# Kernel optimization log

Measured on AMD Instinct MI355X. Metric: run time of the kernel, lower is better.

Reference implementation:

```python
import jax, jax.numpy as jnp
import numpy as np
from functools import partial

EPS = 1e-5
TOP_K = 1
NUM_EXPERTS = 3
LOSS_COEF = 0.01


def conv2d(x, w, stride, pad):
    return jax.lax.conv_general_dilated(
        x, w, (stride, stride), [(pad, pad), (pad, pad)],
        dimension_numbers=("NCHW", "OIHW", "NCHW"))


def setup_inputs() -> dict:
    key = jax.random.key(0)
    ks = jax.random.split(key, 8)
    b, c, t, h, w = 8, 3, 5, 512, 512
    E = NUM_EXPERTS
    s = 0.05  # small init scale
    return {
        "x": jax.random.normal(ks[0], (b, c, t, h, w), jnp.float32),
        "g_conv_w": jax.random.normal(ks[1], (64, 15, 7, 7), jnp.float32) * s,
        "g_bn_gamma": jnp.ones((64,), jnp.float32),
        "g_bn_beta": jnp.zeros((64,), jnp.float32),
        "g_bn_mean": jnp.zeros((64,), jnp.float32),
        "g_bn_var": jnp.ones((64,), jnp.float32),
        "g_fc_w": jax.random.normal(ks[2], (E, 64), jnp.float32) * s,
        "g_fc_b": jnp.zeros((E,), jnp.float32),
        "e_conv1_w": jax.random.normal(ks[3], (E, 64, 15, 7, 7), jnp.float32) * s,
        "e_conv2_w": jax.random.normal(ks[4], (E, 128, 64, 3, 3), jnp.float32) * s,
        "e_head_w1": jax.random.normal(ks[5], (E, 128, 128, 3, 3), jnp.float32) * s,
        "e_head_b1": jnp.zeros((E, 128), jnp.float32),
        "e_head_w2": jax.random.normal(ks[6], (E, 5, 128, 1, 1), jnp.float32) * s,
        "e_head_b2": jnp.zeros((E, 5), jnp.float32),
    }


def gating(xr, g_conv_w, g_bn_gamma, g_bn_beta, g_bn_mean, g_bn_var, g_fc_w, g_fc_b):
    # backbone: conv 7x7 s2 -> BN (eval) -> ReLU -> maxpool 3x3 s2 -> GAP -> fc
    f = conv2d(xr, g_conv_w, 2, 3)
    scale = g_bn_gamma / jnp.sqrt(g_bn_var + EPS)
    f = f * scale[None, :, None, None] + (g_bn_beta - g_bn_mean * scale)[None, :, None, None]
    f = jax.nn.relu(f)
    f = jax.lax.reduce_window(f, -jnp.inf, jax.lax.max, (1, 1, 3, 3), (1, 1, 2, 2),
                              [(0, 0), (0, 0), (1, 1), (1, 1)])
    pooled = f.mean(axis=(2, 3))                       # (b, 64)
    logits = pooled @ g_fc_w.T + g_fc_b                # (b, E)
    b = logits.shape[0]
    _, top_idx = jax.lax.top_k(logits, TOP_K)          # (b, k)
    rows = jnp.arange(b)[:, None]
    # eval-mode gating: uniform 1/k over selected experts
    sparse_gates = jnp.zeros_like(logits).at[rows, top_idx].set(1.0 / TOP_K)
    expert_mask = jnp.zeros_like(logits).at[rows, top_idx].set(1.0)
    density = expert_mask.mean(axis=0)
    density_proxy = jax.nn.softmax(logits, axis=1).mean(axis=0)
    aux_loss = (density * density_proxy).sum() * NUM_EXPERTS
    return sparse_gates, aux_loss


def expert_forward(xr, w1, w2, hw1, hb1, hw2, hb2):
    y = jax.nn.relu(conv2d(xr, w1, 2, 3))              # (b, 64, H/2, W/2)
    y = jax.nn.relu(conv2d(y, w2, 2, 1))               # (b, 128, H/4, W/4)
    y = jax.nn.relu(conv2d(y, hw1, 1, 1) + hb1[None, :, None, None])
    y = conv2d(y, hw2, 1, 0) + hb2[None, :, None, None]  # (b, 5, H/4, W/4)
    return y


def reference(x, g_conv_w, g_bn_gamma, g_bn_beta, g_bn_mean, g_bn_var, g_fc_w, g_fc_b,
              e_conv1_w, e_conv2_w, e_head_w1, e_head_b1, e_head_w2, e_head_b2):
    b, c, t, h, w = x.shape
    xr = x.reshape(b, c * t, h, w)
    sparse_gates, aux_loss = gating(xr, g_conv_w, g_bn_gamma, g_bn_beta,
                                    g_bn_mean, g_bn_var, g_fc_w, g_fc_b)
    # run all experts (gates are 0 for unselected -> identical math to sparse dispatch)
    outs = jax.vmap(lambda w1, w2, hw1, hb1, hw2, hb2:
                    expert_forward(xr, w1, w2, hw1, hb1, hw2, hb2))(
        e_conv1_w, e_conv2_w, e_head_w1, e_head_b1, e_head_w2, e_head_b2)  # (E,b,5,h4,w4)
    combined = jnp.einsum("ebchw,be->bchw", outs, sparse_gates)
    hm, wh, reg = combined[:, 0:1], combined[:, 1:3], combined[:, 3:5]
    return hm, wh, reg, LOSS_COEF * aux_loss
```

## Files before the change

### kernel.cpp

```cpp
#include <hip/hip_runtime.h>
#include <cstdint>
#include <cmath>


typedef _Float16 f16x8 __attribute__((ext_vector_type(8)));
typedef _Float16 f16x4 __attribute__((ext_vector_type(4)));
typedef float f32x4 __attribute__((ext_vector_type(4)));

__device__ __forceinline__ void g2l16(const void* g, void* l) {
  __builtin_amdgcn_global_load_lds((__attribute__((address_space(1))) void*)g,
                                   (__attribute__((address_space(3))) void*)l,
                                   16, 0, 0);
}

__device__ __forceinline__ int xcd_swz(int bid, int nwg) {
  return (bid & 7) * (nwg >> 3) + (bid >> 3);
}

__global__ __launch_bounds__(256) void prep_x_k(
    const float* __restrict__ x, _Float16* __restrict__ xp)
{
  __shared__ __align__(16) _Float16 st[16384];
  const int tid = threadIdx.x;
  const int b   = blockIdx.x >> 8;
  const int blk = blockIdx.x & 255;
  const int px0 = blk * 1024;
  const float* src = x + (size_t)b * 15 * 262144 + px0 + tid * 4;

  f16x8 lo[4], hi[4];
#pragma unroll
  for (int j = 0; j < 4; ++j) hi[j][7] = (_Float16)0.f;
#pragma unroll
  for (int c = 0; c < 15; ++c) {
    const float4 v = *(const float4*)&src[(size_t)c * 262144];
    if (c < 8) {
      lo[0][c] = (_Float16)v.x; lo[1][c] = (_Float16)v.y;
      lo[2][c] = (_Float16)v.z; lo[3][c] = (_Float16)v.w;
    } else {
      hi[0][c - 8] = (_Float16)v.x; hi[1][c - 8] = (_Float16)v.y;
      hi[2][c - 8] = (_Float16)v.z; hi[3][c - 8] = (_Float16)v.w;
    }
  }
#pragma unroll
  for (int j = 0; j < 4; ++j) {
#pragma unroll
    for (int h = 0; h < 2; ++h) {
      const int g  = (tid * 4 + j) * 2 + h;
      const int gs = g ^ ((g >> 3) & 7);
      *(f16x8*)&st[gs * 8] = h ? hi[j] : lo[j];
    }
  }
  __syncthreads();
  _Float16* dst = xp + ((size_t)b * 262144 + px0) * 16;
#pragma unroll
  for (int m = 0; m < 4; ++m) {
    const int px = m * 256 + tid;
#pragma unroll
    for (int h = 0; h < 2; ++h) {
      const int g  = px * 2 + h;
      const int gs = g ^ ((g >> 3) & 7);
      *(f16x8*)&dst[(size_t)px * 16 + h * 8] = *(const f16x8*)&st[gs * 8];
    }
  }
}

__global__ __launch_bounds__(256) void prep_w7_k(
    const float* __restrict__ gw, const float* __restrict__ ew,
    _Float16* __restrict__ wp)
{
  const int i = blockIdx.x * 256 + threadIdx.x;
  const int kk   = i & 31;
  const int cout = (i >> 5) & 63;
  const int pair = (i >> 11) & 3;
  const int v    = i >> 13;
  const int ky = v % 7, set = v / 7;
  const int t = kk >> 4, cin = kk & 15;
  const int kx = 2 * pair + t;
  float val = 0.f;
  if (cin < 15 && kx < 7) {
    if (set == 0) val = gw[((cout * 15 + cin) * 7 + ky) * 7 + kx];
    else          val = ew[((((set - 1) * 64 + cout) * 15 + cin) * 7 + ky) * 7 + kx];
  }
  wp[i] = (_Float16)val;
}

template<int CINC>
__global__ __launch_bounds__(256) void prep_w3_k(
    const float* __restrict__ w, _Float16* __restrict__ wp)
{
  constexpr int CH = CINC / 32;
  const int i = blockIdx.x * 256 + threadIdx.x;
  const int kk   = i & 31;
  const int cout = (i >> 5) & 127;
  int rest = i >> 12;
  const int ch  = rest % CH;  rest /= CH;
  const int tap = rest % 9;
  const int e   = rest / 9;
  const int cin = ch * 32 + kk;
  wp[i] = (_Float16)w[((size_t)(e * 128 + cout) * CINC + cin) * 9 + tap];
}

template<int MODE, int SWZ>
__global__ __launch_bounds__(256, 3) void conv7m_k(
    const _Float16* __restrict__ xp, const _Float16* __restrict__ wp,
    const float* __restrict__ bn_g, const float* __restrict__ bn_b,
    const float* __restrict__ bn_m, const float* __restrict__ bn_v,
    const int* __restrict__ sel, _Float16* __restrict__ out)
{
  constexpr int ROWF = 518 * 16;
  __shared__ __align__(16) _Float16 smem[18432];
  const int sb = SWZ ? xcd_swz(blockIdx.x, 2048) : (int)blockIdx.x;
  const int oy = sb & 255, b = sb >> 8;
  const int wv = threadIdx.x >> 6, lane = threadIdx.x & 63;
  const int ln15 = lane & 15, quad = lane >> 4;
  const int npx0 = wv * 64;

  int set = 0;
  if constexpr (MODE == 1) set = 1 + sel[b];
  const _Float16* wset = wp + (size_t)set * (7 * 4 * 64 * 32);
  const _Float16* xb   = xp + (size_t)b * (512 * 512 * 16);

  const _Float16* xrow[7];
  bool rowok[7];
#pragma unroll
  for (int ky = 0; ky < 7; ++ky) {
    const int iy = 2 * oy - 3 + ky;
    rowok[ky] = (unsigned)iy < 512u;
    const int iyc = iy < 0 ? 0 : (iy > 511 ? 511 : iy);
    xrow[ky] = xb + (size_t)iyc * (512 * 16);
  }

  if (threadIdx.x < 32) {
    const int bi = threadIdx.x >> 4, k = threadIdx.x & 15;
    if (k < 12) {
      const int g = (k < 6) ? k : (1030 + k - 6);
      f16x8 z = {};
      *(f16x8*)&smem[bi * ROWF + g * 8] = z;
    }
  }

  f32x4 acc[4][4];
#pragma unroll
  for (int f = 0; f < 4; ++f)
#pragma unroll
    for (int g = 0; g < 4; ++g) acc[f][g] = (f32x4){0.f, 0.f, 0.f, 0.f};

  auto load_af = [&](int t, f16x8* af) {
    const int ky = t >> 2, pair = t & 3;
    const _Float16* wt = wset + (size_t)((ky * 4 + pair) * 64) * 32;
#pragma unroll
    for (int f = 0; f < 4; ++f)
      af[f] = *(const f16x8*)&wt[(f * 16 + ln15) * 32 + quad * 8];
  };
  auto stage = [&](int ky, int bi) {
    _Float16* bufb = &smem[bi * ROWF];
    const _Float16* xr = xrow[ky];
#pragma unroll
    for (int s = 0; s < 4; ++s) {
      const int seg = wv * 4 + s;
      const int gl = 6 + seg * 64 + lane;
      const int gs = gl ^ ((gl >> 3) & 7);
      g2l16(xr + (size_t)((gs >> 1) - 3) * 16 + (gs & 1) * 8,
            bufb + (6 + seg * 64) * 8);
    }
  };

  int gb[4];
#pragma unroll
  for (int g = 0; g < 4; ++g)
    gb[g] = 4 * (npx0 + g * 16 + ln15) + quad;

  f16x8 afA[4], afB[4];
  load_af(0, afA);
  stage(0, 0);
  __syncthreads();

#pragma unroll
  for (int t = 0; t < 28; ++t) {
    const int ky = t >> 2, pair = t & 3;
    const int cur = ky & 1;
    f16x8* afc = (t & 1) ? afB : afA;
    f16x8* afn = (t & 1) ? afA : afB;
    if (t + 1 < 28) load_af(t + 1, afn);
    if (pair == 0 && ky + 1 < 7) stage(ky + 1, cur ^ 1);
    if (rowok[ky]) {
      const _Float16* bufb = &smem[cur * ROWF];
      __builtin_amdgcn_s_setprio(1);
#pragma unroll
      for (int g = 0; g < 4; ++g) {
        const int gq = gb[g] + 4 * pair;
        const int gs = gq ^ ((gq >> 3) & 7);
        const f16x8 bf = *(const f16x8*)&bufb[gs * 8];
#pragma unroll
        for (int f = 0; f < 4; ++f)
          acc[f][g] = __builtin_amdgcn_mfma_f32_16x16x32_f16(afc[f], bf, acc[f][g], 0, 0, 0);
      }
      __builtin_amdgcn_s_setprio(0);
    }
    if (pair == 3) __syncthreads();
  }

  _Float16* sw = &smem[wv * 4608];
#pragma unroll
  for (int f = 0; f < 4; ++f) {
    float scl[4], add[4];
#pragma unroll
    for (int r = 0; r < 4; ++r) {
      const int cout = f * 16 + quad * 4 + r;
      if constexpr (MODE == 0) {
        const float sc = bn_g[cout] * rsqrtf(bn_v[cout] + 1e-5f);
        scl[r] = sc; add[r] = bn_b[cout] - bn_m[cout] * sc;
      } else { scl[r] = 1.f; add[r] = 0.f; }
    }
#pragma unroll
    for (int g = 0; g < 4; ++g) {
      f16x4 h;
#pragma unroll
      for (int r = 0; r < 4; ++r)
        h[r] = (_Float16)fmaxf(acc[f][g][r] * scl[r] + add[r], 0.f);
      *(f16x4*)&sw[(g * 16 + ln15) * 72 + f * 16 + quad * 4] = h;
    }
  }
  __syncthreads();
  const size_t rowbase = ((size_t)(b * 256 + oy) * 256 + npx0) * 64;
#pragma unroll
  for (int i = 0; i < 8; ++i) {
    const int pxl = (lane >> 3) + i * 8;
    const int c8  = (lane & 7) * 8;
    const f16x8 v = *(const f16x8*)&sw[pxl * 72 + c8];
    *(f16x8*)&out[rowbase + (size_t)pxl * 64 + c8] = v;
  }
}

template<int CINC, int S, int INSZ, int OUTSZ, int MODE>
__global__ __launch_bounds__(256, 3) void conv3m_k(
    const _Float16* __restrict__ xp, const _Float16* __restrict__ wp,
    const float* __restrict__ p_bias, const int* __restrict__ sel,
    _Float16* __restrict__ out)
{
  constexpr int CH  = CINC / 32;
  constexpr int NCH = 3 * CH;
  constexpr int NT  = NCH * 3;
  constexpr int NPX = (S == 1) ? (OUTSZ + 2) : (2 * OUTSZ + 1);
  constexpr int ROWF = NPX * 32;
  constexpr int NGR  = NPX * 4;
  constexpr int SPW  = INSZ / 64;
  constexpr int SMEMF = (4 * ROWF > 18432) ? 4 * ROWF : 18432;
  __shared__ __align__(16) _Float16 smem[SMEMF];
  const int sb = xcd_swz(blockIdx.x, OUTSZ * 8);
  const int oy = sb % OUTSZ, b = sb / OUTSZ;
  const int wv = threadIdx.x >> 6, lane = threadIdx.x & 63;
  const int ln15 = lane & 15, quad = lane >> 4;
  const int mwb = (wv >> 1) * 64, nwb = (wv & 1) * 64;

  const int e = sel[b];
  const _Float16* we = wp + (size_t)e * (9 * CH * 128 * 32);
  const _Float16* xb = xp + (size_t)b * ((size_t)INSZ * INSZ * CINC);

  const _Float16* xrow[3];
  bool rowok[3];
#pragma unroll
  for (int ky = 0; ky < 3; ++ky) {
    const int iy = S * oy + ky - 1;
    rowok[ky] = (unsigned)iy < (unsigned)INSZ;
    const int iyc = iy < 0 ? 0 : (iy >= INSZ ? INSZ - 1 : iy);
    xrow[ky] = xb + (size_t)iyc * INSZ * CINC;
  }

  {
    constexpr int HGPB = (S == 1) ? 8 : 4;
    if (threadIdx.x < 4 * HGPB) {
      const int bi = threadIdx.x / HGPB, k = threadIdx.x % HGPB;
      const int g = (k < 4) ? k : (NGR - 8 + k);
      f16x8 z = {};
      *(f16x8*)&smem[bi * ROWF + g * 8] = z;
    }
  }

  f32x4 acc[4][4];
#pragma unroll
  for (int f = 0; f < 4; ++f)
#pragma unroll
    for (int g = 0; g < 4; ++g) acc[f][g] = (f32x4){0.f, 0.f, 0.f, 0.f};

  auto load_af = [&](int t, f16x8* af) {
    const int c = t / 3, kx = t % 3;
    const int ky = c / CH, ch = c % CH;
    const _Float16* wt = we + (size_t)(((ky * 3 + kx) * CH + ch) * 128) * 32;
#pragma unroll
    for (int f = 0; f < 4; ++f)
      af[f] = *(const f16x8*)&wt[(mwb + f * 16 + ln15) * 32 + quad * 8];
  };
  auto stage = [&](int c, int bi) {
    const int ky = c / CH, ch = c % CH;
    _Float16* bufb = &smem[bi * ROWF];
    const _Float16* xr = xrow[ky];
#pragma unroll
    for (int s = 0; s < SPW; ++s) {
      const int seg = wv * SPW + s;
      const int gl = 4 + seg * 64 + lane;
      const int gs = gl ^ ((gl >> 3) & 7);
      g2l16(xr + (size_t)((gs >> 2) - 1) * CINC + ch * 32 + (gs & 3) * 8,
            bufb + (4 + seg * 64) * 8);
    }
  };

  int gb[4];
#pragma unroll
  for (int g = 0; g < 4; ++g) {
    const int ox = nwb + g * 16 + ln15;
    gb[g] = 4 * S * ox + quad;
  }

  f16x8 afb[3][4];
  load_af(0, afb[0]);
  load_af(1, afb[1]);
  stage(0, 0);
  stage(1, 1);
  __syncthreads();

#pragma unroll
  for (int t = 0; t < NT; ++t) {
    const int c = t / 3, kx = t % 3;
    const int ky = c / CH;
    const int cur = c & 3;
    if (t + 2 < NT) load_af(t + 2, afb[(t + 2) % 3]);
    if (kx == 0 && (c & 1) == 0) {
      if (c + 2 < NCH) stage(c + 2, (c + 2) & 3);
      if (c + 3 < NCH) stage(c + 3, (c + 3) & 3);
    }
    if (rowok[ky]) {
      const _Float16* bufb = &smem[cur * ROWF];
      __builtin_amdgcn_s_setprio(1);
#pragma unroll
      for (int g = 0; g < 4; ++g) {
        const int gq = gb[g] + 4 * kx;
        const int gs = gq ^ ((gq >> 3) & 7);
        const f16x8 bf = *(const f16x8*)&bufb[gs * 8];
#pragma unroll
        for (int f = 0; f < 4; ++f)
          acc[f][g] = __builtin_amdgcn_mfma_f32_16x16x32_f16(afb[t % 3][f], bf, acc[f][g], 0, 0, 0);
      }
      __builtin_amdgcn_s_setprio(0);
    }
    if (kx == 2 && (c & 1)) __syncthreads();
  }

  _Float16* sw = &smem[wv * 4608];
#pragma unroll
  for (int f = 0; f < 4; ++f) {
#pragma unroll
    for (int g = 0; g < 4; ++g) {
      f16x4 h;
#pragma unroll
      for (int r = 0; r < 4; ++r) {
        const int cout = mwb + f * 16 + quad * 4 + r;
        float v = acc[f][g][r];
        if constexpr (MODE == 2) v += p_bias[e * 128 + cout];
        h[r] = (_Float16)fmaxf(v, 0.f);
      }
      *(f16x4*)&sw[(g * 16 + ln15) * 72 + f * 16 + quad * 4] = h;
    }
  }
  __syncthreads();
  const size_t rowbase = ((size_t)(b * OUTSZ + oy) * OUTSZ + nwb) * 128 + mwb;
#pragma unroll
  for (int i = 0; i < 8; ++i) {
    const int pxl = (lane >> 3) + i * 8;
    const int c8  = (lane & 7) * 8;
    const f16x8 v = *(const f16x8*)&sw[pxl * 72 + c8];
    *(f16x8*)&out[rowbase + (size_t)pxl * 128 + c8] = v;
  }
}

__global__ void zero_k(float* __restrict__ pooled) {
  if (threadIdx.x < 512) pooled[threadIdx.x] = 0.f;
}

__global__ __launch_bounds__(256) void pool_k(
    const _Float16* __restrict__ f, float* __restrict__ pooled)
{
  const int sb = xcd_swz(blockIdx.x, 1024);
  const int b  = sb >> 7;
  const int py = sb & 127;
  const int wv = threadIdx.x >> 6, lane = threadIdx.x & 63;
  const int c8  = (lane & 7) * 8;
  const int pxq = lane >> 3;
  const _Float16* fb = f + (size_t)b * 256 * 256 * 64;

  const int y0 = 2 * py - 1;
  float s[8];
#pragma unroll
  for (int j = 0; j < 8; ++j) s[j] = 0.f;

#pragma unroll
  for (int step = 0; step < 4; ++step) {
    const int px = wv * 32 + step * 8 + pxq;
    const int x0 = 2 * px - 1;
    f16x8 m;
#pragma unroll
    for (int j = 0; j < 8; ++j) m[j] = (_Float16)(-60000.f);
#pragma unroll
    for (int dy = 0; dy < 3; ++dy) {
      const int y = y0 + dy;
      if ((unsigned)y < 256u) {
        const _Float16* row = fb + (size_t)y * 256 * 64 + c8;
        if (x0 >= 0)
          m = __builtin_elementwise_max(m, *(const f16x8*)&row[(size_t)x0 * 64]);
        m = __builtin_elementwise_max(m, *(const f16x8*)&row[(size_t)(x0 + 1) * 64]);
        m = __builtin_elementwise_max(m, *(const f16x8*)&row[(size_t)(x0 + 2) * 64]);
      }
    }
#pragma unroll
    for (int j = 0; j < 8; ++j) s[j] += (float)m[j];
  }

  __shared__ float red[256][8];
#pragma unroll
  for (int j = 0; j < 8; ++j) red[threadIdx.x][j] = s[j];
  __syncthreads();
  if (threadIdx.x < 64) {
    const int c = threadIdx.x, cg = c >> 3, cj = c & 7;
    float t = 0.f;
#pragma unroll
    for (int k = 0; k < 32; ++k)
      t += red[(k >> 3) * 64 + (k & 7) * 8 + cg][cj];
    atomicAdd(&pooled[b * 64 + c], t);
  }
}

__global__ __launch_bounds__(64) void gate_k(
    const float* __restrict__ pooled, const float* __restrict__ fcw,
    const float* __restrict__ fcb, int* __restrict__ sel, float* __restrict__ out_aux)
{
  __shared__ float probs[8][3];
  __shared__ int sidx[8];
  const int b = threadIdx.x;
  if (b < 8) {
    float l[3];
#pragma unroll
    for (int e = 0; e < 3; ++e) {
      float s = fcb[e];
      for (int c = 0; c < 64; ++c)
        s = fmaf(pooled[b * 64 + c] * (1.f / 16384.f), fcw[e * 64 + c], s);
      l[e] = s;
    }
    int best = 0;
    if (l[1] > l[best]) best = 1;
    if (l[2] > l[best]) best = 2;
    sel[b] = best;
    sidx[b] = best;
    const float m = fmaxf(l[0], fmaxf(l[1], l[2]));
    const float e0 = expf(l[0] - m), e1 = expf(l[1] - m), e2 = expf(l[2] - m);
    const float inv = 1.f / (e0 + e1 + e2);
    probs[b][0] = e0 * inv; probs[b][1] = e1 * inv; probs[b][2] = e2 * inv;
  }
  __syncthreads();
  if (threadIdx.x == 0) {
    float cnt[3] = {0.f, 0.f, 0.f}, pr[3] = {0.f, 0.f, 0.f};
    for (int bb = 0; bb < 8; ++bb) {
      cnt[sidx[bb]] += 1.f;
#pragma unroll
      for (int e = 0; e < 3; ++e) pr[e] += probs[bb][e];
    }
    float aux = 0.f;
#pragma unroll
    for (int e = 0; e < 3; ++e) aux += (cnt[e] * 0.125f) * (pr[e] * 0.125f);
    *out_aux = 0.01f * (3.f * aux);
  }
}

__global__ __launch_bounds__(256) void head2m_k(
    const _Float16* __restrict__ in, const float* __restrict__ w,
    const float* __restrict__ b2, const int* __restrict__ sel,
    float* __restrict__ out)
{
  const int b = blockIdx.x >> 6;
  const int p = ((blockIdx.x & 63) << 8) + threadIdx.x;
  const int e = sel[b];
  const float* wp = w + (size_t)e * 5 * 128;
  const _Float16* ip = in + ((size_t)(b << 14) + p) * 128;
  float a0 = 0.f, a1 = 0.f, a2 = 0.f, a3 = 0.f, a4 = 0.f;
#pragma unroll
  for (int cc = 0; cc < 16; ++cc) {
    const f16x8 v8 = *(const f16x8*)&ip[cc * 8];
#pragma unroll
    for (int j = 0; j < 8; ++j) {
      const float v = (float)v8[j];
      const int c = cc * 8 + j;
      a0 = fmaf(v, wp[c], a0);
      a1 = fmaf(v, wp[128 + c], a1);
      a2 = fmaf(v, wp[256 + c], a2);
      a3 = fmaf(v, wp[384 + c], a3);
      a4 = fmaf(v, wp[512 + c], a4);
    }
  }
  a0 += b2[e * 5 + 0]; a1 += b2[e * 5 + 1]; a2 += b2[e * 5 + 2];
  a3 += b2[e * 5 + 3]; a4 += b2[e * 5 + 4];
  out[(b << 14) + p] = a0;
  out[131072 + ((b * 2 + 0) << 14) + p] = a1;
  out[131072 + ((b * 2 + 1) << 14) + p] = a2;
  out[393216 + ((b * 2 + 0) << 14) + p] = a3;
  out[393216 + ((b * 2 + 1) << 14) + p] = a4;
}

extern "C" void kernel_launch(void* const* d_in, const int* in_sizes, int n_in,
                              void* d_out, int out_size, void* d_ws, size_t ws_size,
                              hipStream_t stream) {
  const float* x          = (const float*)d_in[0];
  const float* g_conv_w   = (const float*)d_in[1];
  const float* g_bn_gamma = (const float*)d_in[2];
  const float* g_bn_beta  = (const float*)d_in[3];
  const float* g_bn_mean  = (const float*)d_in[4];
  const float* g_bn_var   = (const float*)d_in[5];
  const float* g_fc_w     = (const float*)d_in[6];
  const float* g_fc_b     = (const float*)d_in[7];
  const float* e_conv1_w  = (const float*)d_in[8];
  const float* e_conv2_w  = (const float*)d_in[9];
  const float* e_head_w1  = (const float*)d_in[10];
  const float* e_head_b1  = (const float*)d_in[11];
  const float* e_head_w2  = (const float*)d_in[12];
  const float* e_head_b2  = (const float*)d_in[13];
  float* out = (float*)d_out;

  _Float16* xp      = (_Float16*)d_ws;
  _Float16* featbuf = xp + 33554432;
  _Float16* y2      = featbuf + 33554432;
  _Float16* w7p     = y2 + 16777216;
  _Float16* w2p     = w7p + 229376;
  _Float16* w3p     = w2p + 221184;
  _Float16* y3      = xp;
  float*    pooled  = (float*)(w3p + 442368);
  int*      sel     = (int*)(pooled + 512);

  prep_x_k<<<2048, 256, 0, stream>>>(x, xp);
  prep_w7_k<<<896, 256, 0, stream>>>(g_conv_w, e_conv1_w, w7p);
  prep_w3_k<64><<<864, 256, 0, stream>>>(e_conv2_w, w2p);
  prep_w3_k<128><<<1728, 256, 0, stream>>>(e_head_w1, w3p);
  zero_k<<<1, 512, 0, stream>>>(pooled);

  conv7m_k<0, 1><<<2048, 256, 0, stream>>>(xp, w7p, g_bn_gamma, g_bn_beta,
                                           g_bn_mean, g_bn_var, nullptr, featbuf);
  pool_k<<<1024, 256, 0, stream>>>(featbuf, pooled);
  gate_k<<<1, 64, 0, stream>>>(pooled, g_fc_w, g_fc_b, sel, out + 655360);

  conv7m_k<1, 1><<<2048, 256, 0, stream>>>(xp, w7p, nullptr, nullptr, nullptr, nullptr,
                                           sel, featbuf);
  conv3m_k<64, 2, 256, 128, 1><<<1024, 256, 0, stream>>>(featbuf, w2p, nullptr, sel, y2);
  conv3m_k<128, 1, 128, 128, 2><<<1024, 256, 0, stream>>>(y2, w3p, e_head_b1, sel, y3);
  head2m_k<<<512, 256, 0, stream>>>(y3, e_head_w2, e_head_b2, sel, out);
}
```

Measured before the change: 473.1 us.

## Fuse 1x1 head into head conv epilogue, merge prep kernels, drop setprio

The final 1x1 head convolution (128->5 channels) is now computed in the epilogue of the 3x3 head conv kernel. Each block reduces the ReLU'd accumulators against the expert's head weights, combines partials with lane shuffles and shared memory, and writes the five output planes directly. This removes the round trip of the 128-channel fp16 intermediate through global memory and one kernel launch. The four weight/zero prep kernels are also merged into a single launch, and the s_setprio hints around the MFMA loops are removed. The trade-off is extra scalar FMA and shuffle work plus an added barrier in the conv epilogue.

New measurement: 457.7 us. 1.03x faster.

```diff
diff --git a/kernel.cpp b/kernel.cpp
--- a/kernel.cpp
+++ b/kernel.cpp
@@ -64,40 +64,52 @@
   }
 }
 
-__global__ __launch_bounds__(256) void prep_w7_k(
+__global__ __launch_bounds__(256) void prep_w_k(
     const float* __restrict__ gw, const float* __restrict__ ew,
-    _Float16* __restrict__ wp)
+    const float* __restrict__ w2in, const float* __restrict__ w3in,
+    _Float16* __restrict__ w7p, _Float16* __restrict__ w2p,
+    _Float16* __restrict__ w3p, float* __restrict__ pooled)
 {
-  const int i = blockIdx.x * 256 + threadIdx.x;
-  const int kk   = i & 31;
-  const int cout = (i >> 5) & 63;
-  const int pair = (i >> 11) & 3;
-  const int v    = i >> 13;
-  const int ky = v % 7, set = v / 7;
-  const int t = kk >> 4, cin = kk & 15;
-  const int kx = 2 * pair + t;
-  float val = 0.f;
-  if (cin < 15 && kx < 7) {
-    if (set == 0) val = gw[((cout * 15 + cin) * 7 + ky) * 7 + kx];
-    else          val = ew[((((set - 1) * 64 + cout) * 15 + cin) * 7 + ky) * 7 + kx];
-  }
-  wp[i] = (_Float16)val;
-}
-
-template<int CINC>
-__global__ __launch_bounds__(256) void prep_w3_k(
-    const float* __restrict__ w, _Float16* __restrict__ wp)
-{
-  constexpr int CH = CINC / 32;
-  const int i = blockIdx.x * 256 + threadIdx.x;
-  const int kk   = i & 31;
-  const int cout = (i >> 5) & 127;
-  int rest = i >> 12;
-  const int ch  = rest % CH;  rest /= CH;
-  const int tap = rest % 9;
-  const int e   = rest / 9;
-  const int cin = ch * 32 + kk;
-  wp[i] = (_Float16)w[((size_t)(e * 128 + cout) * CINC + cin) * 9 + tap];
+  const int bid = blockIdx.x;
+  if (bid < 896) {
+    const int i = bid * 256 + threadIdx.x;
+    const int kk   = i & 31;
+    const int cout = (i >> 5) & 63;
+    const int pair = (i >> 11) & 3;
+    const int v    = i >> 13;
+    const int ky = v % 7, set = v / 7;
+    const int t = kk >> 4, cin = kk & 15;
+    const int kx = 2 * pair + t;
+    float val = 0.f;
+    if (cin < 15 && kx < 7) {
+      if (set == 0) val = gw[((cout * 15 + cin) * 7 + ky) * 7 + kx];
+      else          val = ew[((((set - 1) * 64 + cout) * 15 + cin) * 7 + ky) * 7 + kx];
+    }
+    w7p[i] = (_Float16)val;
+  } else if (bid < 1760) {
+    const int i = (bid - 896) * 256 + threadIdx.x;
+    const int kk   = i & 31;
+    const int cout = (i >> 5) & 127;
+    int rest = i >> 12;
+    const int ch  = rest % 2;  rest /= 2;
+    const int tap = rest % 9;
+    const int e   = rest / 9;
+    const int cin = ch * 32 + kk;
+    w2p[i] = (_Float16)w2in[((size_t)(e * 128 + cout) * 64 + cin) * 9 + tap];
+  } else if (bid < 3488) {
+    const int i = (bid - 1760) * 256 + threadIdx.x;
+    const int kk   = i & 31;
+    const int cout = (i >> 5) & 127;
+    int rest = i >> 12;
+    const int ch  = rest % 4;  rest /= 4;
+    const int tap = rest % 9;
+    const int e   = rest / 9;
+    const int cin = ch * 32 + kk;
+    w3p[i] = (_Float16)w3in[((size_t)(e * 128 + cout) * 128 + cin) * 9 + tap];
+  } else {
+    pooled[threadIdx.x]       = 0.f;
+    pooled[256 + threadIdx.x] = 0.f;
+  }
 }
 
 template<int MODE, int SWZ>
@@ -185,7 +197,6 @@
     if (pair == 0 && ky + 1 < 7) stage(ky + 1, cur ^ 1);
     if (rowok[ky]) {
       const _Float16* bufb = &smem[cur * ROWF];
-      __builtin_amdgcn_s_setprio(1);
 #pragma unroll
       for (int g = 0; g < 4; ++g) {
         const int gq = gb[g] + 4 * pair;
@@ -195,7 +206,6 @@
         for (int f = 0; f < 4; ++f)
           acc[f][g] = __builtin_amdgcn_mfma_f32_16x16x32_f16(afc[f], bf, acc[f][g], 0, 0, 0);
       }
-      __builtin_amdgcn_s_setprio(0);
     }
     if (pair == 3) __syncthreads();
   }
@@ -236,7 +246,9 @@
 __global__ __launch_bounds__(256, 3) void conv3m_k(
     const _Float16* __restrict__ xp, const _Float16* __restrict__ wp,
     const float* __restrict__ p_bias, const int* __restrict__ sel,
-    _Float16* __restrict__ out)
+    _Float16* __restrict__ out,
+    const float* __restrict__ hw2, const float* __restrict__ hb2,
+    float* __restrict__ hout)
 {
   constexpr int CH  = CINC / 32;
   constexpr int NCH = 3 * CH;
@@ -331,7 +343,6 @@
     }
     if (rowok[ky]) {
       const _Float16* bufb = &smem[cur * ROWF];
-      __builtin_amdgcn_s_setprio(1);
 #pragma unroll
       for (int g = 0; g < 4; ++g) {
         const int gq = gb[g] + 4 * kx;
@@ -341,40 +352,90 @@
         for (int f = 0; f < 4; ++f)
           acc[f][g] = __builtin_amdgcn_mfma_f32_16x16x32_f16(afb[t % 3][f], bf, acc[f][g], 0, 0, 0);
       }
-      __builtin_amdgcn_s_setprio(0);
     }
     if (kx == 2 && (c & 1)) __syncthreads();
   }
 
-  _Float16* sw = &smem[wv * 4608];
-#pragma unroll
-  for (int f = 0; f < 4; ++f) {
-#pragma unroll
-    for (int g = 0; g < 4; ++g) {
-      f16x4 h;
+  if constexpr (MODE == 2) {
+    float p[4][5];
+#pragma unroll
+    for (int g = 0; g < 4; ++g)
+#pragma unroll
+      for (int oc = 0; oc < 5; ++oc) p[g][oc] = 0.f;
+    const float* w2 = hw2 + (size_t)e * 5 * 128;
+#pragma unroll
+    for (int f = 0; f < 4; ++f) {
 #pragma unroll
       for (int r = 0; r < 4; ++r) {
         const int cout = mwb + f * 16 + quad * 4 + r;
-        float v = acc[f][g][r];
-        if constexpr (MODE == 2) v += p_bias[e * 128 + cout];
-        h[r] = (_Float16)fmaxf(v, 0.f);
+        const float bb = p_bias[e * 128 + cout];
+        float w5[5];
+#pragma unroll
+        for (int oc = 0; oc < 5; ++oc) w5[oc] = w2[oc * 128 + cout];
+#pragma unroll
+        for (int g = 0; g < 4; ++g) {
+          const float v = fmaxf(acc[f][g][r] + bb, 0.f);
+#pragma unroll
+          for (int oc = 0; oc < 5; ++oc) p[g][oc] = fmaf(w5[oc], v, p[g][oc]);
+        }
       }
-      *(f16x4*)&sw[(g * 16 + ln15) * 72 + f * 16 + quad * 4] = h;
-    }
-  }
-  __syncthreads();
-  const size_t rowbase = ((size_t)(b * OUTSZ + oy) * OUTSZ + nwb) * 128 + mwb;
-#pragma unroll
-  for (int i = 0; i < 8; ++i) {
-    const int pxl = (lane >> 3) + i * 8;
-    const int c8  = (lane & 7) * 8;
-    const f16x8 v = *(const f16x8*)&sw[pxl * 72 + c8];
-    *(f16x8*)&out[rowbase + (size_t)pxl * 128 + c8] = v;
-  }
-}
-
-__global__ void zero_k(float* __restrict__ pooled) {
-  if (threadIdx.x < 512) pooled[threadIdx.x] = 0.f;
+    }
+#pragma unroll
+    for (int g = 0; g < 4; ++g)
+#pragma unroll
+      for (int oc = 0; oc < 5; ++oc) {
+        float t0 = p[g][oc];
+        t0 += __shfl_xor(t0, 16);
+        t0 += __shfl_xor(t0, 32);
+        p[g][oc] = t0;
+      }
+    float* sh = (float*)smem;
+    if (quad == 0) {
+#pragma unroll
+      for (int g = 0; g < 4; ++g)
+#pragma unroll
+        for (int oc = 0; oc < 5; ++oc)
+          sh[(wv * 64 + g * 16 + ln15) * 5 + oc] = p[g][oc];
+    }
+    __syncthreads();
+    const int tid = threadIdx.x;
+    if (tid < 128) {
+      const int nw = tid >> 6, idx = tid & 63;
+      float s[5];
+#pragma unroll
+      for (int oc = 0; oc < 5; ++oc)
+        s[oc] = sh[(nw * 64 + idx) * 5 + oc] + sh[((nw + 2) * 64 + idx) * 5 + oc]
+              + hb2[e * 5 + oc];
+      const int pidx = oy * 128 + tid;
+      hout[((size_t)b << 14) + pidx]                       = s[0];
+      hout[131072 + ((size_t)(b * 2 + 0) << 14) + pidx]    = s[1];
+      hout[131072 + ((size_t)(b * 2 + 1) << 14) + pidx]    = s[2];
+      hout[393216 + ((size_t)(b * 2 + 0) << 14) + pidx]    = s[3];
+      hout[393216 + ((size_t)(b * 2 + 1) << 14) + pidx]    = s[4];
+    }
+  } else {
+    _Float16* sw = &smem[wv * 4608];
+#pragma unroll
+    for (int f = 0; f < 4; ++f) {
+#pragma unroll
+      for (int g = 0; g < 4; ++g) {
+        f16x4 h;
+#pragma unroll
+        for (int r = 0; r < 4; ++r)
+          h[r] = (_Float16)fmaxf(acc[f][g][r], 0.f);
+        *(f16x4*)&sw[(g * 16 + ln15) * 72 + f * 16 + quad * 4] = h;
+      }
+    }
+    __syncthreads();
+    const size_t rowbase = ((size_t)(b * OUTSZ + oy) * OUTSZ + nwb) * 128 + mwb;
+#pragma unroll
+    for (int i = 0; i < 8; ++i) {
+      const int pxl = (lane >> 3) + i * 8;
+      const int c8  = (lane & 7) * 8;
+      const f16x8 v = *(const f16x8*)&sw[pxl * 72 + c8];
+      *(f16x8*)&out[rowbase + (size_t)pxl * 128 + c8] = v;
+    }
+  }
 }
 
 __global__ __launch_bounds__(256) void pool_k(
@@ -468,40 +529,6 @@
     for (int e = 0; e < 3; ++e) aux += (cnt[e] * 0.125f) * (pr[e] * 0.125f);
     *out_aux = 0.01f * (3.f * aux);
   }
-}
-
-__global__ __launch_bounds__(256) void head2m_k(
-    const _Float16* __restrict__ in, const float* __restrict__ w,
-    const float* __restrict__ b2, const int* __restrict__ sel,
-    float* __restrict__ out)
-{
-  const int b = blockIdx.x >> 6;
-  const int p = ((blockIdx.x & 63) << 8) + threadIdx.x;
-  const int e = sel[b];
-  const float* wp = w + (size_t)e * 5 * 128;
-  const _Float16* ip = in + ((size_t)(b << 14) + p) * 128;
-  float a0 = 0.f, a1 = 0.f, a2 = 0.f, a3 = 0.f, a4 = 0.f;
-#pragma unroll
-  for (int cc = 0; cc < 16; ++cc) {
-    const f16x8 v8 = *(const f16x8*)&ip[cc * 8];
-#pragma unroll
-    for (int j = 0; j < 8; ++j) {
-      const float v = (float)v8[j];
-      const int c = cc * 8 + j;
-      a0 = fmaf(v, wp[c], a0);
-      a1 = fmaf(v, wp[128 + c], a1);
-      a2 = fmaf(v, wp[256 + c], a2);
-      a3 = fmaf(v, wp[384 + c], a3);
-      a4 = fmaf(v, wp[512 + c], a4);
-    }
-  }
-  a0 += b2[e * 5 + 0]; a1 += b2[e * 5 + 1]; a2 += b2[e * 5 + 2];
-  a3 += b2[e * 5 + 3]; a4 += b2[e * 5 + 4];
-  out[(b << 14) + p] = a0;
-  out[131072 + ((b * 2 + 0) << 14) + p] = a1;
-  out[131072 + ((b * 2 + 1) << 14) + p] = a2;
-  out[393216 + ((b * 2 + 0) << 14) + p] = a3;
-  out[393216 + ((b * 2 + 1) << 14) + p] = a4;
 }
 
 extern "C" void kernel_launch(void* const* d_in, const int* in_sizes, int n_in,
@@ -529,15 +556,12 @@
   _Float16* w7p     = y2 + 16777216;
   _Float16* w2p     = w7p + 229376;
   _Float16* w3p     = w2p + 221184;
-  _Float16* y3      = xp;
   float*    pooled  = (float*)(w3p + 442368);
   int*      sel     = (int*)(pooled + 512);
 
   prep_x_k<<<2048, 256, 0, stream>>>(x, xp);
-  prep_w7_k<<<896, 256, 0, stream>>>(g_conv_w, e_conv1_w, w7p);
-  prep_w3_k<64><<<864, 256, 0, stream>>>(e_conv2_w, w2p);
-  prep_w3_k<128><<<1728, 256, 0, stream>>>(e_head_w1, w3p);
-  zero_k<<<1, 512, 0, stream>>>(pooled);
+  prep_w_k<<<3489, 256, 0, stream>>>(g_conv_w, e_conv1_w, e_conv2_w, e_head_w1,
+                                     w7p, w2p, w3p, pooled);
 
   conv7m_k<0, 1><<<2048, 256, 0, stream>>>(xp, w7p, g_bn_gamma, g_bn_beta,
                                            g_bn_mean, g_bn_var, nullptr, featbuf);
@@ -546,7 +570,8 @@
 
   conv7m_k<1, 1><<<2048, 256, 0, stream>>>(xp, w7p, nullptr, nullptr, nullptr, nullptr,
                                            sel, featbuf);
-  conv3m_k<64, 2, 256, 128, 1><<<1024, 256, 0, stream>>>(featbuf, w2p, nullptr, sel, y2);
-  conv3m_k<128, 1, 128, 128, 2><<<1024, 256, 0, stream>>>(y2, w3p, e_head_b1, sel, y3);
-  head2m_k<<<512, 256, 0, stream>>>(y3, e_head_w2, e_head_b2, sel, out);
-}
+  conv3m_k<64, 2, 256, 128, 1><<<1024, 256, 0, stream>>>(
+      featbuf, w2p, nullptr, sel, y2, nullptr, nullptr, nullptr);
+  conv3m_k<128, 1, 128, 128, 2><<<1024, 256, 0, stream>>>(
+      y2, w3p, e_head_b1, sel, nullptr, e_head_w2, e_head_b2, out);
+}
```
